# Kernel tuning notes

Measured on AMD Instinct MI355X. Metric: run time of the kernel, lower is better.

Reference implementation:

```python
import jax, jax.numpy as jnp
import numpy as np

D = 256          # feature dim per token
DENSE = 1024     # dense_units


def setup_inputs() -> dict:
    key = jax.random.key(0)
    ks = jax.random.split(key, 8)
    f1 = jax.random.normal(ks[0], (256, 128, D), dtype=jnp.float32)
    f2 = jax.random.normal(ks[1], (256, 128, D), dtype=jnp.float32)
    # fc1: Linear(3*D=768 -> DENSE), fc2: DENSE -> DENSE//2, output: DENSE//2 -> 1
    s1 = 1.0 / np.sqrt(3 * D)
    s2 = 1.0 / np.sqrt(DENSE)
    s3 = 1.0 / np.sqrt(DENSE // 2)
    W1 = jax.random.uniform(ks[2], (3 * D, DENSE), jnp.float32, -s1, s1)
    b1 = jax.random.uniform(ks[3], (DENSE,), jnp.float32, -s1, s1)
    W2 = jax.random.uniform(ks[4], (DENSE, DENSE // 2), jnp.float32, -s2, s2)
    b2 = jax.random.uniform(ks[5], (DENSE // 2,), jnp.float32, -s2, s2)
    W3 = jax.random.uniform(ks[6], (DENSE // 2, 1), jnp.float32, -s3, s3)
    b3 = jax.random.uniform(ks[7], (1,), jnp.float32, -s3, s3)
    return {"f1": f1, "f2": f2, "W1": W1, "b1": b1, "W2": W2, "b2": b2,
            "W3": W3, "b3": b3}


def reference(f1, f2, W1, b1, W2, b2, W3, b3):
    N1 = f1.shape[0]
    N2 = f2.shape[0]
    # Mean-pool over L first (algebraically identical to expanding then pooling,
    # avoiding the O(N1*N2*L*D) intermediate the torch code materializes).
    p1 = f1.mean(axis=1)                      # [N1, D]
    p2 = f2.mean(axis=1)                      # [N2, D]
    p1b = jnp.broadcast_to(p1[:, None, :], (N1, N2, D))
    p2b = jnp.broadcast_to(p2[None, :, :], (N1, N2, D))
    combined = jnp.concatenate([p1b, p2b, p1b - p2b], axis=-1)  # [N1, N2, 3D]
    combined = combined.reshape(N1 * N2, 3 * D)
    # Dropout is identity at inference.
    x = jax.nn.gelu(combined @ W1 + b1, approximate=False)
    x = jax.nn.gelu(x @ W2 + b2, approximate=False)
    out = jax.nn.sigmoid(x @ W3 + b3)[:, 0]
    return out.reshape(N1, N2)
```

## Files before the change

kernel.cpp:

```cpp
#include <hip/hip_runtime.h>
#include <hip/hip_bf16.h>


#define N1 256
#define N2 256
#define LTOK 128
#define DDIM 256
#define DENSEU 1024
#define HID 512

typedef float f32x4 __attribute__((ext_vector_type(4)));
typedef short s16x8 __attribute__((ext_vector_type(8)));

__device__ __forceinline__ short f2bf(float x) {
  union { __bf16 b; short s; } cv;
  cv.b = (__bf16)x;
  return cv.s;
}

__device__ __forceinline__ float gelu_fast(float x) {
  float x3 = x * x * x;
  float z = 0.7978845608028654f * (x + 0.044715f * x3);
  float e = __expf(2.0f * z);
  float t = 1.0f - 2.0f / (e + 1.0f);
  return 0.5f * x * (1.0f + t);
}

__global__ void sentinel_kernel(float* out, int n) {
  int i = blockIdx.x * blockDim.x + threadIdx.x;
  if (i < n) out[i] = 123.0f;
}

__global__ __launch_bounds__(256) void pool_kernel(const float* __restrict__ f1,
                                                   const float* __restrict__ f2,
                                                   float* __restrict__ p1,
                                                   float* __restrict__ p2) {
  __shared__ float4 red[256];
  int b = blockIdx.x;
  int tensor = b >> 8;
  int n = b & 255;
  const float* src = tensor ? f2 : f1;
  float* dst = tensor ? p2 : p1;
  int t = threadIdx.x;
  int d4 = (t & 63) * 4;
  int l0 = t >> 6;
  const float4* base = (const float4*)(src + (size_t)n * (LTOK * DDIM) + d4);
  float4 s = {0.f, 0.f, 0.f, 0.f};
  #pragma unroll 8
  for (int l = l0; l < LTOK; l += 4) {
    float4 x = base[l * (DDIM / 4)];
    s.x += x.x; s.y += x.y; s.z += x.z; s.w += x.w;
  }
  red[t] = s;
  __syncthreads();
  if (t < 64) {
    float4 a = red[t], b4 = red[t + 64], c = red[t + 128], d = red[t + 192];
    float4 r;
    r.x = (a.x + b4.x + c.x + d.x) * (1.f / LTOK);
    r.y = (a.y + b4.y + c.y + d.y) * (1.f / LTOK);
    r.z = (a.z + b4.z + c.z + d.z) * (1.f / LTOK);
    r.w = (a.w + b4.w + c.w + d.w) * (1.f / LTOK);
    ((float4*)(dst + (size_t)n * DDIM))[t] = r;
  }
}

__global__ __launch_bounds__(256) void uv_kernel(const float* __restrict__ p1,
                                                 const float* __restrict__ p2,
                                                 const float* __restrict__ W1,
                                                 const float* __restrict__ b1,
                                                 float* __restrict__ u,
                                                 float* __restrict__ v) {
  __shared__ float pl[16][DDIM];
  int t = threadIdx.x;
  int o = blockIdx.x * 256 + t;
  int n0 = blockIdx.y * 16;
  int tensor = blockIdx.z;
  const float* p = tensor ? p2 : p1;
  #pragma unroll
  for (int r = 0; r < 16; ++r) pl[r][t] = p[(size_t)(n0 + r) * DDIM + t];
  __syncthreads();
  const float* wa = W1 + (tensor ? (256 * DENSEU) : 0);
  const float* wc = W1 + 512 * DENSEU;
  float sgn = tensor ? -1.0f : 1.0f;
  float acc[16];
  #pragma unroll
  for (int nn = 0; nn < 16; ++nn) acc[nn] = 0.f;
  for (int d = 0; d < DDIM; ++d) {
    float w = wa[(size_t)d * DENSEU + o] + sgn * wc[(size_t)d * DENSEU + o];
    #pragma unroll
    for (int nn = 0; nn < 16; ++nn) acc[nn] += pl[nn][d] * w;
  }
  float* dst = tensor ? v : u;
  float bb = tensor ? 0.f : b1[o];
  #pragma unroll
  for (int nn = 0; nn < 16; ++nn) dst[(size_t)(n0 + nn) * DENSEU + o] = acc[nn] + bb;
}

__global__ __launch_bounds__(256) void w2t_kernel(const float* __restrict__ W2,
                                                  unsigned short* __restrict__ w2t) {
  __shared__ float tile[32][33];
  int tx = threadIdx.x, ty = threadIdx.y;
  int n0 = blockIdx.x * 32, k0 = blockIdx.y * 32;
  #pragma unroll
  for (int r = 0; r < 4; ++r) {
    int kk = ty + r * 8;
    tile[kk][tx] = W2[(size_t)(k0 + kk) * HID + n0 + tx];
  }
  __syncthreads();
  #pragma unroll
  for (int r = 0; r < 4; ++r) {
    int nn = ty + r * 8;
    w2t[(size_t)(n0 + nn) * DENSEU + k0 + tx] = (unsigned short)f2bf(tile[tx][nn]);
  }
}

__global__ __launch_bounds__(512) void fused_kernel(const float* __restrict__ u,
                                                    const float* __restrict__ v,
                                                    const unsigned short* __restrict__ w2t,
                                                    const float* __restrict__ b2,
                                                    const float* __restrict__ W3,
                                                    const float* __restrict__ b3,
                                                    float* __restrict__ out) {
  __shared__ __align__(16) unsigned char xs[64 * 128];
  __shared__ float rowsum[64];
  int tid = threadIdx.x;
  int lane = tid & 63;
  int wave = tid >> 6;
  int i = blockIdx.x >> 2;
  int j0 = (blockIdx.x & 3) * 64;
  int woff = wave * 64;

  int brow = tid >> 3;
  int bkg = tid & 7;
  const float* urow = u + (size_t)i * DENSEU;
  const float* vrow = v + (size_t)(j0 + brow) * DENSEU;
  unsigned wbyte = (unsigned)(brow * 128) + (((unsigned)bkg << 4) ^ ((unsigned)(brow & 7) << 4));

  unsigned rbase[4], rswz[4];
  #pragma unroll
  for (int mf = 0; mf < 4; ++mf) {
    int r = mf * 16 + (lane & 15);
    rbase[mf] = (unsigned)(r * 128);
    rswz[mf] = (unsigned)((r & 7) << 4);
  }
  unsigned klane = (unsigned)((lane >> 4) << 4);

  int bn[4];
  #pragma unroll
  for (int nf = 0; nf < 4; ++nf) bn[nf] = woff + nf * 16 + (lane & 15);

  f32x4 acc[4][4];
  f32x4 zero = {0.f, 0.f, 0.f, 0.f};
  #pragma unroll
  for (int mf = 0; mf < 4; ++mf)
    #pragma unroll
    for (int nf = 0; nf < 4; ++nf) acc[mf][nf] = zero;

  for (int kt = 0; kt < 16; ++kt) {
    int kkb = kt * 64 + bkg * 8;
    float4 ua = *(const float4*)(urow + kkb);
    float4 ub = *(const float4*)(urow + kkb + 4);
    float4 va = *(const float4*)(vrow + kkb);
    float4 vb = *(const float4*)(vrow + kkb + 4);
    float fv[8] = {ua.x + va.x, ua.y + va.y, ua.z + va.z, ua.w + va.w,
                   ub.x + vb.x, ub.y + vb.y, ub.z + vb.z, ub.w + vb.w};
    s16x8 pk;
    #pragma unroll
    for (int e = 0; e < 8; ++e) pk[e] = f2bf(gelu_fast(fv[e]));
    __syncthreads();
    *(s16x8*)(xs + wbyte) = pk;
    __syncthreads();

    int kglob = kt * 64 + ((lane >> 4) << 3);
    #pragma unroll
    for (int ksub = 0; ksub < 2; ++ksub) {
      s16x8 af[4];
      #pragma unroll
      for (int mf = 0; mf < 4; ++mf) {
        unsigned off = rbase[mf] + ((((unsigned)ksub << 6) | klane) ^ rswz[mf]);
        af[mf] = *(const s16x8*)(xs + off);
      }
      s16x8 bfr[4];
      #pragma unroll
      for (int nf = 0; nf < 4; ++nf)
        bfr[nf] = *(const s16x8*)(w2t + (size_t)bn[nf] * DENSEU + kglob + ksub * 32);
      #pragma unroll
      for (int mf = 0; mf < 4; ++mf)
        #pragma unroll
        for (int nf = 0; nf < 4; ++nf)
          acc[mf][nf] = __builtin_amdgcn_mfma_f32_16x16x32_bf16(af[mf], bfr[nf], acc[mf][nf], 0, 0, 0);
    }
  }

  if (tid < 64) rowsum[tid] = 0.f;
  __syncthreads();
  float b2v[4], w3v[4];
  #pragma unroll
  for (int nf = 0; nf < 4; ++nf) { b2v[nf] = b2[bn[nf]]; w3v[nf] = W3[bn[nf]]; }
  int qr = lane >> 4;
  #pragma unroll
  for (int mf = 0; mf < 4; ++mf) {
    #pragma unroll
    for (int j = 0; j < 4; ++j) {
      float part = 0.f;
      #pragma unroll
      for (int nf = 0; nf < 4; ++nf) {
        float h = acc[mf][nf][j] + b2v[nf];
        part += gelu_fast(h) * w3v[nf];
      }
      part += __shfl_xor(part, 1);
      part += __shfl_xor(part, 2);
      part += __shfl_xor(part, 4);
      part += __shfl_xor(part, 8);
      if ((lane & 15) == 0) atomicAdd(&rowsum[mf * 16 + qr * 4 + j], part);
    }
  }
  __syncthreads();
  if (tid < 64) {
    float s = rowsum[tid] + b3[0];
    out[(size_t)i * N2 + j0 + tid] = 1.0f / (1.0f + __expf(-s));
  }
}

extern "C" void kernel_launch(void* const* d_in, const int* in_sizes, int n_in,
                              void* d_out, int out_size, void* d_ws, size_t ws_size,
                              hipStream_t stream) {
  const float* f1 = (const float*)d_in[0];
  const float* f2 = (const float*)d_in[1];
  const float* W1 = (const float*)d_in[2];
  const float* b1 = (const float*)d_in[3];
  const float* W2 = (const float*)d_in[4];
  const float* b2 = (const float*)d_in[5];
  const float* W3 = (const float*)d_in[6];
  const float* b3 = (const float*)d_in[7];
  float* out = (float*)d_out;

  size_t need_bytes = (size_t)(256 * 256 * 2 + 256 * 1024 * 2) * sizeof(float)
                    + (size_t)(512 * 1024) * sizeof(unsigned short);
  if (n_in < 8 || ws_size < need_bytes) {
    sentinel_kernel<<<(out_size + 255) / 256, 256, 0, stream>>>(out, out_size);
    return;
  }

  float* p1 = (float*)d_ws;
  float* p2 = p1 + 256 * 256;
  float* u  = p2 + 256 * 256;
  float* v  = u + 256 * 1024;
  unsigned short* w2t = (unsigned short*)(v + 256 * 1024);

  pool_kernel<<<512, 256, 0, stream>>>(f1, f2, p1, p2);
  uv_kernel<<<dim3(4, 16, 2), 256, 0, stream>>>(p1, p2, W1, b1, u, v);
  w2t_kernel<<<dim3(16, 32), dim3(32, 8), 0, stream>>>(W2, w2t);
  fused_kernel<<<1024, 512, 0, stream>>>(u, v, w2t, b2, W3, b3, out);
}
```

Baseline: 326.0 us.

## Software-pipeline fused MLP kernel with double-buffered LDS and register prefetch

The fused GEMM loop now double-buffers the GELU'd activation tile in LDS and prefetches the next k-step's W2 fragments into registers. This removes one of the two barriers per k-step and overlaps global loads and GELU math with the MFMAs. The u row is staged once in LDS instead of being reloaded from global memory each step. The GELU is rewritten as x*sigmoid(2z) using a hardware reciprocal, and launch bounds request two blocks per CU. The trade-offs are higher register and LDS pressure and one wasted prefetch on the last iteration.

```diff
diff --git a/kernel.cpp b/kernel.cpp
--- a/kernel.cpp
+++ b/kernel.cpp
@@ -13,17 +13,22 @@
 typedef short s16x8 __attribute__((ext_vector_type(8)));
 
 __device__ __forceinline__ short f2bf(float x) {
-  union { __bf16 b; short s; } cv;
-  cv.b = (__bf16)x;
-  return cv.s;
+  union { __bf16 b; short s; } cv; cv.b = (__bf16)x; return cv.s;
+}
+
+__device__ __forceinline__ float fast_rcp(float x) {
+#if __has_builtin(__builtin_amdgcn_rcpf)
+  return __builtin_amdgcn_rcpf(x);
+#else
+  return 1.0f / x;
+#endif
 }
 
 __device__ __forceinline__ float gelu_fast(float x) {
-  float x3 = x * x * x;
-  float z = 0.7978845608028654f * (x + 0.044715f * x3);
-  float e = __expf(2.0f * z);
-  float t = 1.0f - 2.0f / (e + 1.0f);
-  return 0.5f * x * (1.0f + t);
+  float t = x * x;
+  float z2 = x * fmaf(0.0713548162726f, t, 1.5957691216057308f);
+  float e = __expf(z2);
+  return x * e * fast_rcp(e + 1.0f);
 }
 
 __global__ void sentinel_kernel(float* out, int n) {
@@ -114,89 +119,132 @@
   }
 }
 
-__global__ __launch_bounds__(512) void fused_kernel(const float* __restrict__ u,
-                                                    const float* __restrict__ v,
-                                                    const unsigned short* __restrict__ w2t,
-                                                    const float* __restrict__ b2,
-                                                    const float* __restrict__ W3,
-                                                    const float* __restrict__ b3,
-                                                    float* __restrict__ out) {
-  __shared__ __align__(16) unsigned char xs[64 * 128];
+__global__ __launch_bounds__(512, 2) void fused_kernel(const float* __restrict__ u,
+                                                       const float* __restrict__ v,
+                                                       const unsigned short* __restrict__ w2t,
+                                                       const float* __restrict__ b2,
+                                                       const float* __restrict__ W3,
+                                                       const float* __restrict__ b3,
+                                                       float* __restrict__ out) {
+  __shared__ __align__(16) unsigned char xs[2][64 * 128];
+  __shared__ __align__(16) float u_lds[DENSEU];
   __shared__ float rowsum[64];
-  int tid = threadIdx.x;
-  int lane = tid & 63;
-  int wave = tid >> 6;
-  int i = blockIdx.x >> 2;
-  int j0 = (blockIdx.x & 3) * 64;
-  int woff = wave * 64;
-
-  int brow = tid >> 3;
-  int bkg = tid & 7;
+  const int tid = threadIdx.x;
+  const int lane = tid & 63;
+  const int wave = tid >> 6;
+  const int i = blockIdx.x >> 2;
+  const int j0 = (blockIdx.x & 3) * 64;
+  const int woff = wave * 64;
+  const int brow = tid >> 3;
+  const int bkg = tid & 7;
   const float* urow = u + (size_t)i * DENSEU;
   const float* vrow = v + (size_t)(j0 + brow) * DENSEU;
-  unsigned wbyte = (unsigned)(brow * 128) + (((unsigned)bkg << 4) ^ ((unsigned)(brow & 7) << 4));
-
-  unsigned rbase[4], rswz[4];
+
+  if (tid < 256) ((f32x4*)u_lds)[tid] = ((const f32x4*)urow)[tid];
+  if (tid < 64) rowsum[tid] = 0.f;
+
+  const unsigned wbyte = (unsigned)(brow * 128) +
+                         (((unsigned)bkg << 4) ^ ((unsigned)(brow & 7) << 4));
+  unsigned aoff0[4];
   #pragma unroll
   for (int mf = 0; mf < 4; ++mf) {
     int r = mf * 16 + (lane & 15);
-    rbase[mf] = (unsigned)(r * 128);
-    rswz[mf] = (unsigned)((r & 7) << 4);
-  }
-  unsigned klane = (unsigned)((lane >> 4) << 4);
-
-  int bn[4];
-  #pragma unroll
-  for (int nf = 0; nf < 4; ++nf) bn[nf] = woff + nf * 16 + (lane & 15);
+    aoff0[mf] = (unsigned)(r * 128) +
+                ((((unsigned)(lane >> 4)) << 4) ^ ((unsigned)(r & 7) << 4));
+  }
+  const int kl8 = (lane >> 4) * 8;
+  int bnbase[4];
+  #pragma unroll
+  for (int nf = 0; nf < 4; ++nf) bnbase[nf] = (woff + nf * 16 + (lane & 15)) * DENSEU;
+
+  __syncthreads();
+
+  {
+    float4 va = *(const float4*)(vrow + bkg * 8);
+    float4 vb = *(const float4*)(vrow + bkg * 8 + 4);
+    float4 ua = *(const float4*)(u_lds + bkg * 8);
+    float4 ub = *(const float4*)(u_lds + bkg * 8 + 4);
+    s16x8 pk;
+    pk[0] = f2bf(gelu_fast(ua.x + va.x));
+    pk[1] = f2bf(gelu_fast(ua.y + va.y));
+    pk[2] = f2bf(gelu_fast(ua.z + va.z));
+    pk[3] = f2bf(gelu_fast(ua.w + va.w));
+    pk[4] = f2bf(gelu_fast(ub.x + vb.x));
+    pk[5] = f2bf(gelu_fast(ub.y + vb.y));
+    pk[6] = f2bf(gelu_fast(ub.z + vb.z));
+    pk[7] = f2bf(gelu_fast(ub.w + vb.w));
+    *(s16x8*)(xs[0] + wbyte) = pk;
+  }
+
+  s16x8 bcur[8], bnxt[8];
+  #pragma unroll
+  for (int q = 0; q < 8; ++q)
+    bcur[q] = *(const s16x8*)(w2t + bnbase[q & 3] + (q >> 2) * 32 + kl8);
 
   f32x4 acc[4][4];
-  f32x4 zero = {0.f, 0.f, 0.f, 0.f};
   #pragma unroll
   for (int mf = 0; mf < 4; ++mf)
     #pragma unroll
-    for (int nf = 0; nf < 4; ++nf) acc[mf][nf] = zero;
-
-  for (int kt = 0; kt < 16; ++kt) {
-    int kkb = kt * 64 + bkg * 8;
-    float4 ua = *(const float4*)(urow + kkb);
-    float4 ub = *(const float4*)(urow + kkb + 4);
-    float4 va = *(const float4*)(vrow + kkb);
-    float4 vb = *(const float4*)(vrow + kkb + 4);
-    float fv[8] = {ua.x + va.x, ua.y + va.y, ua.z + va.z, ua.w + va.w,
-                   ub.x + vb.x, ub.y + vb.y, ub.z + vb.z, ub.w + vb.w};
-    s16x8 pk;
-    #pragma unroll
-    for (int e = 0; e < 8; ++e) pk[e] = f2bf(gelu_fast(fv[e]));
-    __syncthreads();
-    *(s16x8*)(xs + wbyte) = pk;
-    __syncthreads();
-
-    int kglob = kt * 64 + ((lane >> 4) << 3);
-    #pragma unroll
-    for (int ksub = 0; ksub < 2; ++ksub) {
-      s16x8 af[4];
-      #pragma unroll
-      for (int mf = 0; mf < 4; ++mf) {
-        unsigned off = rbase[mf] + ((((unsigned)ksub << 6) | klane) ^ rswz[mf]);
-        af[mf] = *(const s16x8*)(xs + off);
-      }
-      s16x8 bfr[4];
-      #pragma unroll
-      for (int nf = 0; nf < 4; ++nf)
-        bfr[nf] = *(const s16x8*)(w2t + (size_t)bn[nf] * DENSEU + kglob + ksub * 32);
-      #pragma unroll
-      for (int mf = 0; mf < 4; ++mf)
-        #pragma unroll
-        for (int nf = 0; nf < 4; ++nf)
-          acc[mf][nf] = __builtin_amdgcn_mfma_f32_16x16x32_bf16(af[mf], bfr[nf], acc[mf][nf], 0, 0, 0);
+    for (int nf = 0; nf < 4; ++nf) {
+      f32x4 z = {0.f, 0.f, 0.f, 0.f};
+      acc[mf][nf] = z;
     }
-  }
-
-  if (tid < 64) rowsum[tid] = 0.f;
-  __syncthreads();
+
+  __syncthreads();
+
+#define KSTEP(KT, RB, WB, BC, BN_)                                            \
+  {                                                                           \
+    const int ktn = ((KT) + 1) & 15;                                          \
+    const int kb = ktn * 64 + bkg * 8;                                        \
+    float4 va = *(const float4*)(vrow + kb);                                  \
+    float4 vb = *(const float4*)(vrow + kb + 4);                              \
+    _Pragma("unroll")                                                         \
+    for (int q = 0; q < 8; ++q)                                               \
+      BN_[q] = *(const s16x8*)(w2t + bnbase[q & 3] + ktn * 64 + (q >> 2) * 32 + kl8); \
+    s16x8 af[8];                                                              \
+    _Pragma("unroll")                                                         \
+    for (int mf = 0; mf < 4; ++mf) {                                          \
+      af[mf] = *(const s16x8*)(xs[RB] + aoff0[mf]);                           \
+      af[4 + mf] = *(const s16x8*)(xs[RB] + (aoff0[mf] ^ 64));                \
+    }                                                                         \
+    _Pragma("unroll")                                                         \
+    for (int mf = 0; mf < 4; ++mf)                                            \
+      _Pragma("unroll")                                                       \
+      for (int nf = 0; nf < 4; ++nf)                                          \
+        acc[mf][nf] = __builtin_amdgcn_mfma_f32_16x16x32_bf16(af[mf], BC[nf], acc[mf][nf], 0, 0, 0); \
+    _Pragma("unroll")                                                         \
+    for (int mf = 0; mf < 4; ++mf)                                            \
+      _Pragma("unroll")                                                       \
+      for (int nf = 0; nf < 4; ++nf)                                          \
+        acc[mf][nf] = __builtin_amdgcn_mfma_f32_16x16x32_bf16(af[4 + mf], BC[4 + nf], acc[mf][nf], 0, 0, 0); \
+    float4 ua = *(const float4*)(u_lds + kb);                                 \
+    float4 ub = *(const float4*)(u_lds + kb + 4);                             \
+    s16x8 pk;                                                                 \
+    pk[0] = f2bf(gelu_fast(ua.x + va.x));                                     \
+    pk[1] = f2bf(gelu_fast(ua.y + va.y));                                     \
+    pk[2] = f2bf(gelu_fast(ua.z + va.z));                                     \
+    pk[3] = f2bf(gelu_fast(ua.w + va.w));                                     \
+    pk[4] = f2bf(gelu_fast(ub.x + vb.x));                                     \
+    pk[5] = f2bf(gelu_fast(ub.y + vb.y));                                     \
+    pk[6] = f2bf(gelu_fast(ub.z + vb.z));                                     \
+    pk[7] = f2bf(gelu_fast(ub.w + vb.w));                                     \
+    *(s16x8*)(xs[WB] + wbyte) = pk;                                           \
+    __syncthreads();                                                          \
+  }
+
+  for (int kt2 = 0; kt2 < 8; ++kt2) {
+    KSTEP(kt2 * 2, 0, 1, bcur, bnxt)
+    KSTEP(kt2 * 2 + 1, 1, 0, bnxt, bcur)
+  }
+#undef KSTEP
+
   float b2v[4], w3v[4];
   #pragma unroll
-  for (int nf = 0; nf < 4; ++nf) { b2v[nf] = b2[bn[nf]]; w3v[nf] = W3[bn[nf]]; }
+  for (int nf = 0; nf < 4; ++nf) {
+    int bnn = woff + nf * 16 + (lane & 15);
+    b2v[nf] = b2[bnn];
+    w3v[nf] = W3[bnn];
+  }
   int qr = lane >> 4;
   #pragma unroll
   for (int mf = 0; mf < 4; ++mf) {
@@ -218,7 +266,7 @@
   __syncthreads();
   if (tid < 64) {
     float s = rowsum[tid] + b3[0];
-    out[(size_t)i * N2 + j0 + tid] = 1.0f / (1.0f + __expf(-s));
+    out[(size_t)i * N2 + j0 + tid] = fast_rcp(1.0f + __expf(-s));
   }
 }
 
```

New measurement: 304.1 us. -6.7%, faster.
